# Optimization experiments

Hardware: AMD Instinct MI355X
Metric: run time of the kernel (lower is better)

The kernel has to match this reference:

```python
import jax, jax.numpy as jnp
import numpy as np

N = 100000
E = 1600000
F_IN = 128
DIM = 32
NUM_CLASSES = 40
BN_EPS = 1e-5


def setup_inputs() -> dict:
    key = jax.random.key(0)
    ks = jax.random.split(key, 16)
    inp = {}
    inp['x'] = jax.random.normal(ks[0], (N, F_IN), dtype=jnp.float32)
    inp['edge_index'] = jax.random.randint(ks[1], (2, E), 0, N, dtype=jnp.int64)
    s = lambda fan_in: 1.0 / np.sqrt(fan_in)
    # GINConv 1 MLP: Linear(F_IN, DIM) -> ReLU -> Linear(DIM, DIM)
    inp['w1a'] = jax.random.uniform(ks[2], (F_IN, DIM), jnp.float32, -s(F_IN), s(F_IN))
    inp['b1a'] = jnp.zeros((DIM,), jnp.float32)
    inp['w1b'] = jax.random.uniform(ks[3], (DIM, DIM), jnp.float32, -s(DIM), s(DIM))
    inp['b1b'] = jnp.zeros((DIM,), jnp.float32)
    # GINConv 2 MLP: Linear(DIM, DIM) -> ReLU -> Linear(DIM, DIM)
    inp['w2a'] = jax.random.uniform(ks[4], (DIM, DIM), jnp.float32, -s(DIM), s(DIM))
    inp['b2a'] = jnp.zeros((DIM,), jnp.float32)
    inp['w2b'] = jax.random.uniform(ks[5], (DIM, DIM), jnp.float32, -s(DIM), s(DIM))
    inp['b2b'] = jnp.zeros((DIM,), jnp.float32)
    # BatchNorm params (eval mode: running stats)
    inp['bn1_g'] = jnp.ones((DIM,), jnp.float32)
    inp['bn1_b'] = jnp.zeros((DIM,), jnp.float32)
    inp['bn1_m'] = jax.random.normal(ks[6], (DIM,), jnp.float32) * 0.1
    inp['bn1_v'] = jax.random.uniform(ks[7], (DIM,), jnp.float32, 0.5, 1.5)
    inp['bn2_g'] = jnp.ones((DIM,), jnp.float32)
    inp['bn2_b'] = jnp.zeros((DIM,), jnp.float32)
    inp['bn2_m'] = jax.random.normal(ks[8], (DIM,), jnp.float32) * 0.1
    inp['bn2_v'] = jax.random.uniform(ks[9], (DIM,), jnp.float32, 0.5, 1.5)
    # FC heads
    inp['fc1_w'] = jax.random.uniform(ks[10], (DIM, DIM), jnp.float32, -s(DIM), s(DIM))
    inp['fc1_b'] = jnp.zeros((DIM,), jnp.float32)
    inp['fc2_w'] = jax.random.uniform(ks[11], (DIM, NUM_CLASSES), jnp.float32, -s(DIM), s(DIM))
    inp['fc2_b'] = jnp.zeros((NUM_CLASSES,), jnp.float32)
    return inp


def _gin_conv(x, src, dst, wa, ba, wb, bb):
    # sum-aggregate neighbor features (messages flow src -> dst), eps = 0
    agg = jax.ops.segment_sum(x[src], dst, num_segments=N)
    h = agg + x  # (1 + eps) * x + sum_j x_j
    h = jax.nn.relu(h @ wa + ba)
    return h @ wb + bb


def _bn(x, g, b, m, v):
    return (x - m) * (g * jax.lax.rsqrt(v + BN_EPS)) + b


def reference(x, edge_index, w1a, b1a, w1b, b1b, w2a, b2a, w2b, b2b,
              bn1_g, bn1_b, bn1_m, bn1_v, bn2_g, bn2_b, bn2_m, bn2_v,
              fc1_w, fc1_b, fc2_w, fc2_b):
    src, dst = edge_index[0], edge_index[1]
    h = jax.nn.relu(_gin_conv(x, src, dst, w1a, b1a, w1b, b1b))
    h = _bn(h, bn1_g, bn1_b, bn1_m, bn1_v)  # dropout is identity in eval
    h = _gin_conv(h, src, dst, w2a, b2a, w2b, b2b)
    h = _bn(h, bn2_g, bn2_b, bn2_m, bn2_v)
    h = jax.nn.relu(h @ fc1_w + fc1_b)
    logits = h @ fc2_w + fc2_b
    return jax.nn.log_softmax(logits, axis=1)
```

## Files before the change

kernel.cpp:

```cpp
#include <hip/hip_runtime.h>
#include <hip/hip_bf16.h>

static constexpr int N_   = 100000;
static constexpr int E_   = 1600000;
static constexpr int FIN_ = 128;
static constexpr int DIM_ = 32;
static constexpr int NC_  = 40;
static constexpr int NB_BKT = (N_ + 127) / 128;
static constexpr int NCHUNK = 512;
static constexpr int EPC    = E_ / NCHUNK;

__global__ void detect_kernel(const void* __restrict__ edge, int* __restrict__ flag) {
    if (blockIdx.x == 0 && threadIdx.x == 0) {
        const long long* p = (const long long*)edge;
        int ok = 1;
        for (int i = 0; i < 64; ++i) {
            long long v = p[i];
            if (v < 0 || v >= (long long)N_) { ok = 0; break; }
        }
        *flag = ok;
    }
}

__device__ __forceinline__ int edge_at(const void* e, int is64, long long i) {
    return is64 ? (int)((const long long*)e)[i] : ((const int*)e)[i];
}

__device__ __forceinline__ float bflo(unsigned u) { return __uint_as_float(u << 16); }
__device__ __forceinline__ float bfhi(unsigned u) { return __uint_as_float(u & 0xffff0000u); }

__global__ __launch_bounds__(256) void chist_kernel(const void* __restrict__ edge,
                                                    const int* __restrict__ flag,
                                                    int* __restrict__ ghist) {
    __shared__ int lh[NB_BKT];
    for (int i = threadIdx.x; i < NB_BKT; i += 256) lh[i] = 0;
    __syncthreads();
    int f = *flag;
    int b = blockIdx.x;
    int end = b * EPC + EPC;
    for (int e = b * EPC + threadIdx.x; e < end; e += 256) {
        int d = edge_at(edge, f, (long long)E_ + e);
        atomicAdd(&lh[d >> 7], 1);
    }
    __syncthreads();
    for (int i = threadIdx.x; i < NB_BKT; i += 256) ghist[b * NB_BKT + i] = lh[i];
}

__global__ __launch_bounds__(512) void colscan_kernel(const int* __restrict__ ghist,
                                                      int* __restrict__ gcurT,
                                                      int* __restrict__ bcnt) {
    __shared__ int a[NCHUNK];
    int k = blockIdx.x, tid = threadIdx.x;
    int v = ghist[tid * NB_BKT + k];
    a[tid] = v;
    __syncthreads();
    for (int off = 1; off < NCHUNK; off <<= 1) {
        int t = a[tid] + ((tid >= off) ? a[tid - off] : 0);
        __syncthreads();
        a[tid] = t;
        __syncthreads();
    }
    gcurT[k * NCHUNK + tid] = a[tid] - v;
    if (tid == NCHUNK - 1) bcnt[k] = a[tid];
}

__global__ __launch_bounds__(1024) void bscan_kernel(const int* __restrict__ bcnt,
                                                     int* __restrict__ bbase,
                                                     int* __restrict__ offs) {
    __shared__ int a[1024];
    int tid = threadIdx.x;
    int v = (tid < NB_BKT) ? bcnt[tid] : 0;
    a[tid] = v;
    __syncthreads();
    for (int off = 1; off < 1024; off <<= 1) {
        int t = a[tid] + ((tid >= off) ? a[tid - off] : 0);
        __syncthreads();
        a[tid] = t;
        __syncthreads();
    }
    if (tid < NB_BKT) bbase[tid] = a[tid] - v;
    if (tid == NB_BKT - 1) offs[N_] = a[tid];
}

__global__ __launch_bounds__(256) void dscatter_kernel(const void* __restrict__ edge,
                                                       const int* __restrict__ flag,
                                                       const int* __restrict__ bbase,
                                                       const int* __restrict__ gcurT,
                                                       int* __restrict__ packed) {
    __shared__ int cur[NB_BKT];
    int b = blockIdx.x, tid = threadIdx.x;
    for (int k = tid; k < NB_BKT; k += 256) cur[k] = bbase[k] + gcurT[k * NCHUNK + b];
    __syncthreads();
    int f = *flag;
    int end = b * EPC + EPC;
    for (int e = b * EPC + tid; e < end; e += 256) {
        int s = edge_at(edge, f, e);
        int d = edge_at(edge, f, (long long)E_ + e);
        int pos = atomicAdd(&cur[d >> 7], 1);
        packed[pos] = s | ((d & 127) << 17);
    }
}

__global__ __launch_bounds__(256) void bsort_kernel(const int* __restrict__ bcnt,
                                                    const int* __restrict__ bbase,
                                                    const int* __restrict__ packed,
                                                    int* __restrict__ offs,
                                                    int* __restrict__ csr) {
    __shared__ int c[128];
    __shared__ int cur[128];
    int tid = threadIdx.x;
    int b = blockIdx.x;
    int beg = bbase[b], cnt = bcnt[b];
    if (tid < 128) c[tid] = 0;
    __syncthreads();
    for (int i = tid; i < cnt; i += 256)
        atomicAdd(&c[packed[beg + i] >> 17], 1);
    __syncthreads();
    int myv = (tid < 128) ? c[tid] : 0;
    for (int off = 1; off < 128; off <<= 1) {
        int t = 0;
        if (tid < 128) t = c[tid] + ((tid >= off) ? c[tid - off] : 0);
        __syncthreads();
        if (tid < 128) c[tid] = t;
        __syncthreads();
    }
    if (tid < 128) {
        int ex = c[tid] - myv;
        cur[tid] = ex;
        int node = b * 128 + tid;
        if (node < N_) offs[node] = beg + ex;
    }
    __syncthreads();
    for (int i = tid; i < cnt; i += 256) {
        int v = packed[beg + i];
        int p = atomicAdd(&cur[v >> 17], 1);
        csr[beg + p] = v & 0x1FFFF;
    }
}

__global__ __launch_bounds__(256) void proj1_kernel(const float* __restrict__ x,
                                                    const float* __restrict__ w,
                                                    __hip_bfloat16* __restrict__ yh) {
    __shared__ float wsm[FIN_ * DIM_];
    __shared__ float xs[32][FIN_];
    int tid = threadIdx.x;

    const float4* w4 = (const float4*)w;
    float4* ws4 = (float4*)wsm;
    for (int i = tid; i < FIN_ * DIM_ / 4; i += 256) ws4[i] = w4[i];

    int nodeBase = blockIdx.x * 32;
    const float4* x4 = (const float4*)(x + (size_t)nodeBase * FIN_);
    float4* xs4 = (float4*)&xs[0][0];
    for (int i = tid; i < 32 * FIN_ / 4; i += 256) xs4[i] = x4[i];
    __syncthreads();

    int d = tid & 31, ns = tid >> 5;
    for (int rep = 0; rep < 4; ++rep) {
        int node = ns + rep * 8;
        float acc = 0.f;
#pragma unroll 4
        for (int k = 0; k < FIN_; ++k) acc += xs[node][k] * wsm[k * DIM_ + d];
        yh[(size_t)(nodeBase + node) * DIM_ + d] = __float2bfloat16(acc);
    }
}

__global__ __launch_bounds__(256) void aggmlp1_kernel(const int* __restrict__ offs,
                                                      const int* __restrict__ csr,
                                                      const __hip_bfloat16* __restrict__ yh,
                                                      const float* __restrict__ b1a,
                                                      const float* __restrict__ w1b,
                                                      const float* __restrict__ b1b,
                                                      const float* __restrict__ g1,
                                                      const float* __restrict__ be1,
                                                      const float* __restrict__ m1,
                                                      const float* __restrict__ v1,
                                                      const float* __restrict__ w2a,
                                                      __hip_bfloat16* __restrict__ zh) {
    __shared__ float A[32 * 33];
    __shared__ float B[32 * 33];
    __shared__ float w1s[DIM_ * DIM_];
    __shared__ float w2s[DIM_ * DIM_];
    int tid = threadIdx.x;
    for (int i = tid; i < DIM_ * DIM_; i += 256) { w1s[i] = w1b[i]; w2s[i] = w2a[i]; }

    int nl = tid >> 3, lane = tid & 7;
    int node = blockIdx.x * 32 + nl;
    int beg = offs[node], end = offs[node + 1];
    float a0 = 0.f, a1 = 0.f, a2 = 0.f, a3 = 0.f;
    const char* vb = (const char*)yh;
    int loff = lane << 3;
    int i = beg;
    for (; i + 1 < end; i += 2) {
        int s0 = csr[i], s1 = csr[i + 1];
        uint2 u0 = *(const uint2*)(vb + (((size_t)s0) << 6) + loff);
        uint2 u1 = *(const uint2*)(vb + (((size_t)s1) << 6) + loff);
        a0 += bflo(u0.x) + bflo(u1.x); a1 += bfhi(u0.x) + bfhi(u1.x);
        a2 += bflo(u0.y) + bflo(u1.y); a3 += bfhi(u0.y) + bfhi(u1.y);
    }
    if (i < end) {
        int s0 = csr[i];
        uint2 u0 = *(const uint2*)(vb + (((size_t)s0) << 6) + loff);
        a0 += bflo(u0.x); a1 += bfhi(u0.x); a2 += bflo(u0.y); a3 += bfhi(u0.y);
    }
    {
        float* p = &A[nl * 33 + lane * 4];
        p[0] = a0; p[1] = a1; p[2] = a2; p[3] = a3;
    }
    __syncthreads();

    int d = tid & 31, ng = tid >> 5;
    size_t gbase = (size_t)blockIdx.x * 32 * DIM_;

#pragma unroll
    for (int r = 0; r < 4; ++r) {
        int n = r * 8 + ng;
        float yv = __bfloat162float(yh[gbase + n * DIM_ + d]);
        A[n * 33 + d] = fmaxf(A[n * 33 + d] + yv + b1a[d], 0.f);
    }
    __syncthreads();

    float sc1 = g1[d] * rsqrtf(v1[d] + 1e-5f);
    float sh1 = be1[d] - m1[d] * sc1;

#pragma unroll
    for (int r = 0; r < 4; ++r) {
        int n = r * 8 + ng;
        float acc = b1b[d];
#pragma unroll
        for (int k = 0; k < DIM_; ++k) acc += A[n * 33 + k] * w1s[k * DIM_ + d];
        B[n * 33 + d] = fmaxf(acc, 0.f) * sc1 + sh1;
    }
    __syncthreads();

#pragma unroll
    for (int r = 0; r < 4; ++r) {
        int n = r * 8 + ng;
        float acc = 0.f;
#pragma unroll
        for (int k = 0; k < DIM_; ++k) acc += B[n * 33 + k] * w2s[k * DIM_ + d];
        zh[gbase + n * DIM_ + d] = __float2bfloat16(acc);
    }
}

__global__ __launch_bounds__(256) void aggmlp2_kernel(const int* __restrict__ offs,
                                                      const int* __restrict__ csr,
                                                      const __hip_bfloat16* __restrict__ zh,
                                                      const float* __restrict__ b2a,
                                                      const float* __restrict__ w2b,
                                                      const float* __restrict__ b2b,
                                                      const float* __restrict__ g2,
                                                      const float* __restrict__ be2,
                                                      const float* __restrict__ m2,
                                                      const float* __restrict__ v2,
                                                      const float* __restrict__ f1w,
                                                      const float* __restrict__ f1b,
                                                      const float* __restrict__ f2w,
                                                      const float* __restrict__ f2b,
                                                      float* __restrict__ out) {
    __shared__ float A[32 * 33];
    __shared__ float B[32 * 33];
    __shared__ float wA[DIM_ * DIM_];
    __shared__ float wB[DIM_ * DIM_];
    __shared__ float wC[DIM_ * NC_];
    int tid = threadIdx.x;
    for (int i = tid; i < DIM_ * DIM_; i += 256) { wA[i] = w2b[i]; wB[i] = f1w[i]; }
    for (int i = tid; i < DIM_ * NC_; i += 256) wC[i] = f2w[i];

    int nl = tid >> 3, lane = tid & 7;
    int node = blockIdx.x * 32 + nl;
    int beg = offs[node], end = offs[node + 1];
    float a0 = 0.f, a1 = 0.f, a2 = 0.f, a3 = 0.f;
    const char* vb = (const char*)zh;
    int loff = lane << 3;
    int i = beg;
    for (; i + 1 < end; i += 2) {
        int s0 = csr[i], s1 = csr[i + 1];
        uint2 u0 = *(const uint2*)(vb + (((size_t)s0) << 6) + loff);
        uint2 u1 = *(const uint2*)(vb + (((size_t)s1) << 6) + loff);
        a0 += bflo(u0.x) + bflo(u1.x); a1 += bfhi(u0.x) + bfhi(u1.x);
        a2 += bflo(u0.y) + bflo(u1.y); a3 += bfhi(u0.y) + bfhi(u1.y);
    }
    if (i < end) {
        int s0 = csr[i];
        uint2 u0 = *(const uint2*)(vb + (((size_t)s0) << 6) + loff);
        a0 += bflo(u0.x); a1 += bfhi(u0.x); a2 += bflo(u0.y); a3 += bfhi(u0.y);
    }
    {
        float* p = &A[nl * 33 + lane * 4];
        p[0] = a0; p[1] = a1; p[2] = a2; p[3] = a3;
    }
    __syncthreads();

    int d = tid & 31, ng = tid >> 5;
    size_t gbase = (size_t)blockIdx.x * 32 * DIM_;

#pragma unroll
    for (int r = 0; r < 4; ++r) {
        int n = r * 8 + ng;
        float zv = __bfloat162float(zh[gbase + n * DIM_ + d]);
        A[n * 33 + d] = fmaxf(A[n * 33 + d] + zv + b2a[d], 0.f);
    }
    __syncthreads();

    float sc2 = g2[d] * rsqrtf(v2[d] + 1e-5f);
    float sh2 = be2[d] - m2[d] * sc2;

#pragma unroll
    for (int r = 0; r < 4; ++r) {
        int n = r * 8 + ng;
        float acc = b2b[d];
#pragma unroll
        for (int k = 0; k < DIM_; ++k) acc += A[n * 33 + k] * wA[k * DIM_ + d];
        B[n * 33 + d] = acc * sc2 + sh2;
    }
    __syncthreads();

#pragma unroll
    for (int r = 0; r < 4; ++r) {
        int n = r * 8 + ng;
        float acc = f1b[d];
#pragma unroll
        for (int k = 0; k < DIM_; ++k) acc += B[n * 33 + k] * wB[k * DIM_ + d];
        A[n * 33 + d] = fmaxf(acc, 0.f);
    }
    __syncthreads();

    int c2 = 32 + (d & 7);
#pragma unroll
    for (int r = 0; r < 4; ++r) {
        int n = r * 8 + ng;
        float l0 = f2b[d];
        float l1 = f2b[c2];
#pragma unroll
        for (int k = 0; k < DIM_; ++k) {
            float fv = A[n * 33 + k];
            l0 += fv * wC[k * NC_ + d];
            l1 += fv * wC[k * NC_ + c2];
        }
        float mx = fmaxf(l0, l1);
#pragma unroll
        for (int off = 16; off; off >>= 1) mx = fmaxf(mx, __shfl_xor(mx, off));
        float se = __expf(l0 - mx) + ((d < 8) ? __expf(l1 - mx) : 0.f);
#pragma unroll
        for (int off = 16; off; off >>= 1) se += __shfl_xor(se, off);
        float lse = mx + __logf(se);
        size_t ob = (size_t)(blockIdx.x * 32 + n) * NC_;
        out[ob + d] = l0 - lse;
        if (d < 8) out[ob + 32 + d] = l1 - lse;
    }
}

extern "C" void kernel_launch(void* const* d_in, const int* in_sizes, int n_in,
                              void* d_out, int out_size, void* d_ws, size_t ws_size,
                              hipStream_t stream) {
    const float* x   = (const float*)d_in[0];
    const void*  edg = d_in[1];
    const float* w1a = (const float*)d_in[2];
    const float* b1a = (const float*)d_in[3];
    const float* w1b = (const float*)d_in[4];
    const float* b1b = (const float*)d_in[5];
    const float* w2a = (const float*)d_in[6];
    const float* b2a = (const float*)d_in[7];
    const float* w2b = (const float*)d_in[8];
    const float* b2b = (const float*)d_in[9];
    const float* g1  = (const float*)d_in[10];
    const float* be1 = (const float*)d_in[11];
    const float* m1  = (const float*)d_in[12];
    const float* v1  = (const float*)d_in[13];
    const float* g2  = (const float*)d_in[14];
    const float* be2 = (const float*)d_in[15];
    const float* m2  = (const float*)d_in[16];
    const float* v2  = (const float*)d_in[17];
    const float* f1w = (const float*)d_in[18];
    const float* f1b = (const float*)d_in[19];
    const float* f2w = (const float*)d_in[20];
    const float* f2b = (const float*)d_in[21];
    float* out = (float*)d_out;

    char* ws = (char*)d_ws;
    int* flag   = (int*)ws;
    int* bcnt   = (int*)(ws + 256);
    int* bbase  = (int*)(ws + 3584);
    int* ghist  = (int*)(ws + 6912);
    int* gcurT  = (int*)(ws + 1608448);
    int* offs   = (int*)(ws + 3209984);
    int* packed = (int*)(ws + 3610112);
    int* csr    = (int*)(ws + 10010112);
    __hip_bfloat16* yh = (__hip_bfloat16*)(ws + 16410112);
    __hip_bfloat16* zh = (__hip_bfloat16*)(ws + 22810112);

    detect_kernel<<<1, 64, 0, stream>>>(edg, flag);

    chist_kernel<<<NCHUNK, 256, 0, stream>>>(edg, flag, ghist);
    colscan_kernel<<<NB_BKT, NCHUNK, 0, stream>>>(ghist, gcurT, bcnt);
    bscan_kernel<<<1, 1024, 0, stream>>>(bcnt, bbase, offs);
    dscatter_kernel<<<NCHUNK, 256, 0, stream>>>(edg, flag, bbase, gcurT, packed);
    bsort_kernel<<<NB_BKT, 256, 0, stream>>>(bcnt, bbase, packed, offs, csr);

    proj1_kernel<<<N_ / 32, 256, 0, stream>>>(x, w1a, yh);
    aggmlp1_kernel<<<N_ / 32, 256, 0, stream>>>(offs, csr, yh, b1a, w1b, b1b,
                                                g1, be1, m1, v1, w2a, zh);

    aggmlp2_kernel<<<N_ / 32, 256, 0, stream>>>(offs, csr, zh, b2a, w2b, b2b,
                                                g2, be2, m2, v2, f1w, f1b, f2w, f2b, out);
}
```

Measured before the change: 357.1 us.

## Halve chunk count, unroll neighbor gather by four, reuse shared buffer in aggmlp2

Halves the number of edge chunks in the CSR build, so the histogram and column-scan arrays shrink and fewer blocks and scan steps are needed. Each chunk block now processes twice as many edges. The neighbor gather is factored into a helper that issues four row loads per iteration instead of two, for more memory-level parallelism. aggmlp2 reuses one shared buffer for the intermediate activations and the fc2 weights, cutting LDS use at the cost of an extra barrier. The detect kernel uses a wave ballot instead of a serial loop.

Result: faster. 329.7 us (-7.7%).

```diff
diff --git a/kernel.cpp b/kernel.cpp
--- a/kernel.cpp
+++ b/kernel.cpp
@@ -7,18 +7,16 @@
 static constexpr int DIM_ = 32;
 static constexpr int NC_  = 40;
 static constexpr int NB_BKT = (N_ + 127) / 128;
-static constexpr int NCHUNK = 512;
+static constexpr int NCHUNK = 256;
 static constexpr int EPC    = E_ / NCHUNK;
 
 __global__ void detect_kernel(const void* __restrict__ edge, int* __restrict__ flag) {
-    if (blockIdx.x == 0 && threadIdx.x == 0) {
+    if (blockIdx.x == 0) {
         const long long* p = (const long long*)edge;
-        int ok = 1;
-        for (int i = 0; i < 64; ++i) {
-            long long v = p[i];
-            if (v < 0 || v >= (long long)N_) { ok = 0; break; }
-        }
-        *flag = ok;
+        long long v = p[threadIdx.x & 63];
+        bool bad = (v < 0 || v >= (long long)N_);
+        unsigned long long m = __ballot(bad);
+        if (threadIdx.x == 0) *flag = (m == 0ull) ? 1 : 0;
     }
 }
 
@@ -46,9 +44,9 @@
     for (int i = threadIdx.x; i < NB_BKT; i += 256) ghist[b * NB_BKT + i] = lh[i];
 }
 
-__global__ __launch_bounds__(512) void colscan_kernel(const int* __restrict__ ghist,
-                                                      int* __restrict__ gcurT,
-                                                      int* __restrict__ bcnt) {
+__global__ __launch_bounds__(NCHUNK) void colscan_kernel(const int* __restrict__ ghist,
+                                                         int* __restrict__ gcurT,
+                                                         int* __restrict__ bcnt) {
     __shared__ int a[NCHUNK];
     int k = blockIdx.x, tid = threadIdx.x;
     int v = ghist[tid * NB_BKT + k];
@@ -162,6 +160,29 @@
 #pragma unroll 4
         for (int k = 0; k < FIN_; ++k) acc += xs[node][k] * wsm[k * DIM_ + d];
         yh[(size_t)(nodeBase + node) * DIM_ + d] = __float2bfloat16(acc);
+    }
+}
+
+__device__ __forceinline__ void gather_row(const int* __restrict__ csr,
+                                           const char* __restrict__ vb,
+                                           int beg, int end, int loff,
+                                           float& a0, float& a1, float& a2, float& a3) {
+    int i = beg;
+    for (; i + 3 < end; i += 4) {
+        int s0 = csr[i], s1 = csr[i + 1], s2 = csr[i + 2], s3 = csr[i + 3];
+        uint2 u0 = *(const uint2*)(vb + (((size_t)s0) << 6) + loff);
+        uint2 u1 = *(const uint2*)(vb + (((size_t)s1) << 6) + loff);
+        uint2 u2 = *(const uint2*)(vb + (((size_t)s2) << 6) + loff);
+        uint2 u3 = *(const uint2*)(vb + (((size_t)s3) << 6) + loff);
+        a0 += (bflo(u0.x) + bflo(u1.x)) + (bflo(u2.x) + bflo(u3.x));
+        a1 += (bfhi(u0.x) + bfhi(u1.x)) + (bfhi(u2.x) + bfhi(u3.x));
+        a2 += (bflo(u0.y) + bflo(u1.y)) + (bflo(u2.y) + bflo(u3.y));
+        a3 += (bfhi(u0.y) + bfhi(u1.y)) + (bfhi(u2.y) + bfhi(u3.y));
+    }
+    for (; i < end; ++i) {
+        int s0 = csr[i];
+        uint2 u0 = *(const uint2*)(vb + (((size_t)s0) << 6) + loff);
+        a0 += bflo(u0.x); a1 += bfhi(u0.x); a2 += bflo(u0.y); a3 += bfhi(u0.y);
     }
 }
 
@@ -188,21 +209,7 @@
     int node = blockIdx.x * 32 + nl;
     int beg = offs[node], end = offs[node + 1];
     float a0 = 0.f, a1 = 0.f, a2 = 0.f, a3 = 0.f;
-    const char* vb = (const char*)yh;
-    int loff = lane << 3;
-    int i = beg;
-    for (; i + 1 < end; i += 2) {
-        int s0 = csr[i], s1 = csr[i + 1];
-        uint2 u0 = *(const uint2*)(vb + (((size_t)s0) << 6) + loff);
-        uint2 u1 = *(const uint2*)(vb + (((size_t)s1) << 6) + loff);
-        a0 += bflo(u0.x) + bflo(u1.x); a1 += bfhi(u0.x) + bfhi(u1.x);
-        a2 += bflo(u0.y) + bflo(u1.y); a3 += bfhi(u0.y) + bfhi(u1.y);
-    }
-    if (i < end) {
-        int s0 = csr[i];
-        uint2 u0 = *(const uint2*)(vb + (((size_t)s0) << 6) + loff);
-        a0 += bflo(u0.x); a1 += bfhi(u0.x); a2 += bflo(u0.y); a3 += bfhi(u0.y);
-    }
+    gather_row(csr, (const char*)yh, beg, end, lane << 3, a0, a1, a2, a3);
     {
         float* p = &A[nl * 33 + lane * 4];
         p[0] = a0; p[1] = a1; p[2] = a2; p[3] = a3;
@@ -259,33 +266,17 @@
                                                       const float* __restrict__ f2b,
                                                       float* __restrict__ out) {
     __shared__ float A[32 * 33];
-    __shared__ float B[32 * 33];
+    __shared__ float BC[DIM_ * NC_];
     __shared__ float wA[DIM_ * DIM_];
     __shared__ float wB[DIM_ * DIM_];
-    __shared__ float wC[DIM_ * NC_];
     int tid = threadIdx.x;
     for (int i = tid; i < DIM_ * DIM_; i += 256) { wA[i] = w2b[i]; wB[i] = f1w[i]; }
-    for (int i = tid; i < DIM_ * NC_; i += 256) wC[i] = f2w[i];
 
     int nl = tid >> 3, lane = tid & 7;
     int node = blockIdx.x * 32 + nl;
     int beg = offs[node], end = offs[node + 1];
     float a0 = 0.f, a1 = 0.f, a2 = 0.f, a3 = 0.f;
-    const char* vb = (const char*)zh;
-    int loff = lane << 3;
-    int i = beg;
-    for (; i + 1 < end; i += 2) {
-        int s0 = csr[i], s1 = csr[i + 1];
-        uint2 u0 = *(const uint2*)(vb + (((size_t)s0) << 6) + loff);
-        uint2 u1 = *(const uint2*)(vb + (((size_t)s1) << 6) + loff);
-        a0 += bflo(u0.x) + bflo(u1.x); a1 += bfhi(u0.x) + bfhi(u1.x);
-        a2 += bflo(u0.y) + bflo(u1.y); a3 += bfhi(u0.y) + bfhi(u1.y);
-    }
-    if (i < end) {
-        int s0 = csr[i];
-        uint2 u0 = *(const uint2*)(vb + (((size_t)s0) << 6) + loff);
-        a0 += bflo(u0.x); a1 += bfhi(u0.x); a2 += bflo(u0.y); a3 += bfhi(u0.y);
-    }
+    gather_row(csr, (const char*)zh, beg, end, lane << 3, a0, a1, a2, a3);
     {
         float* p = &A[nl * 33 + lane * 4];
         p[0] = a0; p[1] = a1; p[2] = a2; p[3] = a3;
@@ -312,7 +303,7 @@
         float acc = b2b[d];
 #pragma unroll
         for (int k = 0; k < DIM_; ++k) acc += A[n * 33 + k] * wA[k * DIM_ + d];
-        B[n * 33 + d] = acc * sc2 + sh2;
+        BC[n * 33 + d] = acc * sc2 + sh2;
     }
     __syncthreads();
 
@@ -321,9 +312,11 @@
         int n = r * 8 + ng;
         float acc = f1b[d];
 #pragma unroll
-        for (int k = 0; k < DIM_; ++k) acc += B[n * 33 + k] * wB[k * DIM_ + d];
+        for (int k = 0; k < DIM_; ++k) acc += BC[n * 33 + k] * wB[k * DIM_ + d];
         A[n * 33 + d] = fmaxf(acc, 0.f);
     }
+    __syncthreads();
+    for (int i = tid; i < DIM_ * NC_; i += 256) BC[i] = f2w[i];
     __syncthreads();
 
     int c2 = 32 + (d & 7);
@@ -335,8 +328,8 @@
 #pragma unroll
         for (int k = 0; k < DIM_; ++k) {
             float fv = A[n * 33 + k];
-            l0 += fv * wC[k * NC_ + d];
-            l1 += fv * wC[k * NC_ + c2];
+            l0 += fv * BC[k * NC_ + d];
+            l1 += fv * BC[k * NC_ + c2];
         }
         float mx = fmaxf(l0, l1);
 #pragma unroll
@@ -383,12 +376,12 @@
     int* bcnt   = (int*)(ws + 256);
     int* bbase  = (int*)(ws + 3584);
     int* ghist  = (int*)(ws + 6912);
-    int* gcurT  = (int*)(ws + 1608448);
-    int* offs   = (int*)(ws + 3209984);
-    int* packed = (int*)(ws + 3610112);
-    int* csr    = (int*)(ws + 10010112);
-    __hip_bfloat16* yh = (__hip_bfloat16*)(ws + 16410112);
-    __hip_bfloat16* zh = (__hip_bfloat16*)(ws + 22810112);
+    int* gcurT  = (int*)(ws + 807680);
+    int* offs   = (int*)(ws + 1608448);
+    int* packed = (int*)(ws + 2008576);
+    int* csr    = (int*)(ws + 8408576);
+    __hip_bfloat16* yh = (__hip_bfloat16*)(ws + 14808576);
+    __hip_bfloat16* zh = (__hip_bfloat16*)(ws + 21208576);
 
     detect_kernel<<<1, 64, 0, stream>>>(edg, flag);
 
```
